# Kernel optimization log

Measured on AMD Instinct MI355X. Metric: run time of the kernel, lower is better.

Reference implementation:

```python
import jax, jax.numpy as jnp
import numpy as np
from jax.ops import segment_sum

B = 4096      # graphs per side (= batch of triples)
NPG = 32      # nodes per graph
N = B * NPG   # total nodes per batched graph
EPG = 128     # edges per graph
E = B * EPG   # total edges per batched graph
D = 256       # emb_dim
D4 = D // 4   # gnn1 out dim


def setup_inputs() -> dict:
    key = jax.random.key(0)
    ks = jax.random.split(key, 16)
    base = jnp.repeat(jnp.arange(B, dtype=jnp.int32) * NPG, EPG)  # graph offsets per edge
    def edges(k1, k2):
        s = base + jax.random.randint(k1, (E,), 0, NPG, dtype=jnp.int32)
        d = base + jax.random.randint(k2, (E,), 0, NPG, dtype=jnp.int32)
        return s, d
    subj_src, subj_dst = edges(ks[0], ks[1])
    obj_src, obj_dst = edges(ks[2], ks[3])
    node_graph_ids = jnp.repeat(jnp.arange(B, dtype=jnp.int32), NPG)
    # negative sampling indices (precomputed randomness, as in _sample_batch_negative_triples)
    head_or_tail = jax.random.randint(ks[4], (B,), 0, 2, dtype=jnp.int32)
    random_rows = jax.random.permutation(ks[5], B).astype(jnp.int32)
    ar = jnp.arange(B, dtype=jnp.int32)
    corrupt_hidx = jnp.where(head_or_tail == 1, random_rows, ar)
    corrupt_tidx = jnp.where(head_or_tail == 0, random_rows, ar)
    s = 0.02
    p = lambda k, sh: jax.random.normal(k, sh, dtype=jnp.float32) * s
    return {
        "subj_node_embs": jax.random.normal(ks[6], (N, D), dtype=jnp.float32),
        "obj_node_embs": jax.random.normal(ks[7], (N, D), dtype=jnp.float32),
        "rel_tok_embs": jax.random.normal(ks[8], (B, D), dtype=jnp.float32),
        "subj_src": subj_src, "subj_dst": subj_dst,
        "obj_src": obj_src, "obj_dst": obj_dst,
        "node_graph_ids": node_graph_ids,
        "corrupt_hidx": corrupt_hidx, "corrupt_tidx": corrupt_tidx,
        "WO1": p(ks[9], (D4, D)), "bO1": jnp.zeros((D4,), jnp.float32),
        "WI1": p(ks[10], (D4, D)), "bI1": jnp.zeros((D4,), jnp.float32),
        "WO2": p(ks[11], (D, D4)), "bO2": jnp.zeros((D,), jnp.float32),
        "WI2": p(ks[12], (D, D4)), "bI2": jnp.zeros((D,), jnp.float32),
        "relW": p(ks[13], (D, D)), "relb": jnp.zeros((D,), jnp.float32),
    }


def _mean_agg(h, idx_from, idx_to, n):
    # mean over edges (idx_from -> idx_to) of h[idx_from], per destination node; 0 for isolated
    deg = segment_sum(jnp.ones((idx_from.shape[0],), h.dtype), idx_to, num_segments=n)
    s = segment_sum(jnp.take(h, idx_from, axis=0), idx_to, num_segments=n)
    return s / jnp.maximum(deg, 1.0)[:, None]


def _compgcn(src, dst, h, WO, bO, WI, bI):
    n = h.shape[0]
    ho = _mean_agg(h, src, dst, n)   # forward graph: mean of in-neighbor sources
    hi = _mean_agg(h, dst, src, n)   # reversed graph: mean of out-neighbor targets
    return (ho @ WO.T + bO) + (hi @ WI.T + bI)


def _graph_emb(src, dst, node_embs, gids, WO1, bO1, WI1, bI1, WO2, bO2, WI2, bI2):
    hn = jax.nn.relu(_compgcn(src, dst, node_embs, WO1, bO1, WI1, bI1))
    hn = jax.nn.relu(_compgcn(src, dst, hn, WO2, bO2, WI2, bI2))
    # mean readout per graph
    cnt = segment_sum(jnp.ones((hn.shape[0],), hn.dtype), gids, num_segments=B)
    return segment_sum(hn, gids, num_segments=B) / cnt[:, None]


def _dist(h, r, t):
    return jnp.linalg.norm(h + r - t, ord=2, axis=1)


def reference(subj_node_embs, obj_node_embs, rel_tok_embs,
              subj_src, subj_dst, obj_src, obj_dst, node_graph_ids,
              corrupt_hidx, corrupt_tidx,
              WO1, bO1, WI1, bI1, WO2, bO2, WI2, bI2, relW, relb):
    h_embs = _graph_emb(subj_src, subj_dst, subj_node_embs, node_graph_ids,
                        WO1, bO1, WI1, bI1, WO2, bO2, WI2, bI2)
    t_embs = _graph_emb(obj_src, obj_dst, obj_node_embs, node_graph_ids,
                        WO1, bO1, WI1, bI1, WO2, bO2, WI2, bI2)
    r_embs = jax.nn.relu(rel_tok_embs @ relW.T + relb)
    pos_scores = _dist(h_embs, r_embs, t_embs)
    neg_scores = _dist(h_embs[corrupt_hidx], r_embs, t_embs[corrupt_tidx])
    return pos_scores, neg_scores
```

## Files before the change

kernel.cpp:

```cpp
#include <hip/hip_runtime.h>
#include <hip/hip_bf16.h>

#define BGR 4096
#define DIM 256
#define NGPB 8
#define HS  257

typedef __bf16 bf16x8 __attribute__((ext_vector_type(8)));
typedef __bf16 bf16x4 __attribute__((ext_vector_type(4)));
typedef float  f32x4  __attribute__((ext_vector_type(4)));

typedef const __attribute__((address_space(1))) unsigned int* gas_u32p;
typedef __attribute__((address_space(3))) unsigned int* las_u32p;

__device__ __forceinline__ unsigned short f2b(float f) {
  unsigned u = __builtin_bit_cast(unsigned, f);
  u = (u + 0x7FFFu + ((u >> 16) & 1u)) >> 16;
  return (unsigned short)u;
}

__device__ __forceinline__ bf16x8 cvt8(float4 a, float4 b) {
  bf16x8 r;
  r[0] = (__bf16)a.x; r[1] = (__bf16)a.y; r[2] = (__bf16)a.z; r[3] = (__bf16)a.w;
  r[4] = (__bf16)b.x; r[5] = (__bf16)b.y; r[6] = (__bf16)b.z; r[7] = (__bf16)b.w;
  return r;
}
__device__ __forceinline__ bf16x4 cvt4(f32x4 c) {
  bf16x4 r;
  r[0] = (__bf16)c[0]; r[1] = (__bf16)c[1]; r[2] = (__bf16)c[2]; r[3] = (__bf16)c[3];
  return r;
}

__global__ void wcvt_kernel(
    const float* __restrict__ WO1, const float* __restrict__ WI1,
    const float* __restrict__ WO2, const float* __restrict__ WI2,
    const float* __restrict__ bO1, const float* __restrict__ bI1,
    const float* __restrict__ bO2, const float* __restrict__ bI2,
    unsigned short* __restrict__ W1b, unsigned short* __restrict__ W2b,
    float* __restrict__ b1, float* __restrict__ b2)
{
  const int i = blockIdx.x * 256 + threadIdx.x;
  { int j = i >> 8, k = i & 255;
    float v = (j < 64) ? WO1[j * 256 + k] : WI1[(j - 64) * 256 + k];
    W1b[i] = f2b(v); }
  { int j = i >> 7, k = i & 127;
    float v = (k < 64) ? WO2[j * 64 + k] : WI2[j * 64 + (k - 64)];
    W2b[i] = f2b(v); }
  if (i < 64)  b1[i] = bO1[i] + bI1[i];
  if (i < 256) b2[i] = bO2[i] + bI2[i];
}

__global__ __launch_bounds__(256)
__attribute__((amdgpu_waves_per_eu(1, 2)))
void gemm0_kernel(
    const float* __restrict__ subj, const float* __restrict__ obj,
    const unsigned short* __restrict__ W1b, unsigned short* __restrict__ Yt)
{
  __shared__ __align__(16) float S[2][32 * 256];
  const int t = threadIdx.x, w = t >> 6, l = t & 63;
  const int ln16 = l & 15, kg = l >> 4;
  const int gid0 = blockIdx.x * NGPB;

  auto STAGE = [&](int g, int buf) {
    const int gid = gid0 + g;
    const float* Eg = ((gid >> 12) ? obj : subj) + (size_t)(gid & (BGR - 1)) * 32 * DIM;
    #pragma unroll
    for (int i = 0; i < 8; i++) {
      const int r = w * 8 + i;
      const float* src = Eg + r * 256 + ((l ^ i) << 2);
      __builtin_amdgcn_global_load_lds((gas_u32p)(const void*)src,
                                       (las_u32p)(void*)(&S[buf][r * 256]), 16, 0, 0);
    }
  };

  STAGE(0, 0);
  bf16x8 B0[8], B1[8];
  {
    const unsigned short* wb0 = W1b + ((2 * w) * 16 + ln16) * 256 + kg * 8;
    const unsigned short* wb1 = W1b + ((2 * w + 1) * 16 + ln16) * 256 + kg * 8;
    #pragma unroll
    for (int ks = 0; ks < 8; ks++) {
      B0[ks] = *(const bf16x8*)(wb0 + ks * 32);
      B1[ks] = *(const bf16x8*)(wb1 + ks * 32);
    }
  }
  STAGE(1, 1);

  #pragma unroll
  for (int g = 0; g < NGPB; g++) {
    if (g + 1 < NGPB) { asm volatile("s_waitcnt vmcnt(8)" ::: "memory"); }
    else              { asm volatile("s_waitcnt vmcnt(0)" ::: "memory"); }
    __builtin_amdgcn_s_barrier();
    __builtin_amdgcn_sched_barrier(0);

    const float* eb = &S[g & 1][0];
    const int swz = ln16 & 7;
    f32x4 a00 = {0,0,0,0}, a01 = {0,0,0,0}, a10 = {0,0,0,0}, a11 = {0,0,0,0};
    #pragma unroll
    for (int ks = 0; ks < 8; ks++) {
      const int c0 = ks * 8 + kg * 2;
      float4 lo0 = *(const float4*)(eb + ln16 * 256 + ((c0 ^ swz) << 2));
      float4 hi0 = *(const float4*)(eb + ln16 * 256 + (((c0 + 1) ^ swz) << 2));
      bf16x8 A0 = cvt8(lo0, hi0);
      a00 = __builtin_amdgcn_mfma_f32_16x16x32_bf16(A0, B0[ks], a00, 0, 0, 0);
      a01 = __builtin_amdgcn_mfma_f32_16x16x32_bf16(A0, B1[ks], a01, 0, 0, 0);
      float4 lo1 = *(const float4*)(eb + (16 + ln16) * 256 + ((c0 ^ swz) << 2));
      float4 hi1 = *(const float4*)(eb + (16 + ln16) * 256 + (((c0 + 1) ^ swz) << 2));
      bf16x8 A1 = cvt8(lo1, hi1);
      a10 = __builtin_amdgcn_mfma_f32_16x16x32_bf16(A1, B0[ks], a10, 0, 0, 0);
      a11 = __builtin_amdgcn_mfma_f32_16x16x32_bf16(A1, B1[ks], a11, 0, 0, 0);
    }
    {
      const int gid = gid0 + g;
      unsigned short* yo = Yt + (size_t)gid * 4096 + kg * 4;
      *(bf16x4*)(yo + ((2 * w) * 16 + ln16) * 32)          = cvt4(a00);
      *(bf16x4*)(yo + ((2 * w + 1) * 16 + ln16) * 32)      = cvt4(a01);
      *(bf16x4*)(yo + ((2 * w) * 16 + ln16) * 32 + 16)     = cvt4(a10);
      *(bf16x4*)(yo + ((2 * w + 1) * 16 + ln16) * 32 + 16) = cvt4(a11);
    }

    __builtin_amdgcn_sched_barrier(0);
    __builtin_amdgcn_s_barrier();
    __builtin_amdgcn_sched_barrier(0);
    if (g + 2 < NGPB) STAGE(g + 2, g & 1);
  }
}

__global__ __launch_bounds__(256)
__attribute__((amdgpu_waves_per_eu(2, 3)))
void graph_bc_kernel(
    const unsigned short* __restrict__ Yt,
    const int* __restrict__ ssrc, const int* __restrict__ sdst,
    const int* __restrict__ osrc, const int* __restrict__ odst,
    const unsigned short* __restrict__ W2b,
    const float* __restrict__ b1, const float* __restrict__ b2,
    float* __restrict__ gout)
{
  __shared__ __align__(16) unsigned char S[53248];
  const int t = threadIdx.x, w = t >> 6, l = t & 63;
  const int ln16 = l & 15, kg = l >> 4;
  const int gid = blockIdx.x * 4 + w;
  const int side = gid >> 12, g = gid & (BGR - 1);
  unsigned char* h1t = S + w * 13312;
  unsigned char* a2  = S + w * 13312 + 4608;
  unsigned* cw = (unsigned*)a2;

  const int* __restrict__ srcp = side ? osrc : ssrc;
  const int* __restrict__ dstp = side ? odst : sdst;

  const int eb = g * 128 + l;
  const int s0 = srcp[eb] & 31, s1 = srcp[eb + 64] & 31;
  const int d0 = dstp[eb] & 31, d1 = dstp[eb + 64] & 31;

  const unsigned short* yg = Yt + (size_t)gid * 4096;
  bf16x8 Bo[4], Bi[4];
  #pragma unroll
  for (int nt = 0; nt < 4; nt++) {
    Bo[nt] = *(const bf16x8*)(yg + (nt * 16 + ln16) * 32 + kg * 8);
    Bi[nt] = *(const bf16x8*)(yg + (64 + nt * 16 + ln16) * 32 + kg * 8);
  }
  float b1j[4];
  #pragma unroll
  for (int nt = 0; nt < 4; nt++) b1j[nt] = b1[nt * 16 + ln16];

  #pragma unroll
  for (int i = 0; i < 5; i++) cw[l + i * 64] = 0u;
  atomicAdd(&cw[d0 * 8 + (s0 >> 2)], 1u << ((s0 & 3) * 8));
  atomicAdd(&cw[d1 * 8 + (s1 >> 2)], 1u << ((s1 & 3) * 8));
  atomicAdd(&cw[256 + d0], 1u); atomicAdd(&cw[256 + d1], 1u);
  atomicAdd(&cw[288 + s0], 1u); atomicAdd(&cw[288 + s1], 1u);

  bf16x8 m1f[2], m2f[2];
  #pragma unroll
  for (int hf = 0; hf < 2; hf++) {
    const int r = hf * 16 + ln16;
    const float fi = 1.0f / fmaxf((float)cw[256 + r], 1.0f);
    const float fo = 1.0f / fmaxf((float)cw[288 + r], 1.0f);
    const unsigned w0 = cw[r * 8 + kg * 2], w1 = cw[r * 8 + kg * 2 + 1];
    bf16x8 a, b;
    #pragma unroll
    for (int q = 0; q < 4; q++) {
      a[q]     = (__bf16)((float)((w0 >> (q * 8)) & 255u) * fi);
      a[4 + q] = (__bf16)((float)((w1 >> (q * 8)) & 255u) * fi);
    }
    #pragma unroll
    for (int q = 0; q < 8; q++) {
      const unsigned wq = cw[(kg * 8 + q) * 8 + (r >> 2)];
      b[q] = (__bf16)((float)((wq >> ((r & 3) * 8)) & 255u) * fo);
    }
    m1f[hf] = a; m2f[hf] = b;
  }

  #pragma unroll
  for (int mt = 0; mt < 2; mt++)
    #pragma unroll
    for (int nt = 0; nt < 4; nt++) {
      f32x4 z = {0.f, 0.f, 0.f, 0.f};
      f32x4 c = __builtin_amdgcn_mfma_f32_16x16x32_bf16(m1f[mt], Bo[nt], z, 0, 0, 0);
      c = __builtin_amdgcn_mfma_f32_16x16x32_bf16(m2f[mt], Bi[nt], c, 0, 0, 0);
      f32x4 hv = { fmaxf(c[0] + b1j[nt], 0.f), fmaxf(c[1] + b1j[nt], 0.f),
                   fmaxf(c[2] + b1j[nt], 0.f), fmaxf(c[3] + b1j[nt], 0.f) };
      *(bf16x4*)(h1t + (nt * 16 + ln16) * 72 + (mt * 16 + kg * 4) * 2) = cvt4(hv);
    }

  #pragma unroll
  for (int mta = 0; mta < 4; mta++) {
    bf16x8 Af = *(const bf16x8*)(h1t + (mta * 16 + ln16) * 72 + kg * 16);
    #pragma unroll
    for (int hf = 0; hf < 2; hf++)
      #pragma unroll
      for (int ntd = 0; ntd < 2; ntd++) {
        f32x4 z = {0.f, 0.f, 0.f, 0.f};
        f32x4 c = __builtin_amdgcn_mfma_f32_16x16x32_bf16(
            Af, hf ? m2f[ntd] : m1f[ntd], z, 0, 0, 0);
        *(bf16x4*)(a2 + (ntd * 16 + ln16) * 272 + hf * 128 + mta * 32 + kg * 8) = cvt4(c);
      }
  }

  bf16x8 BF[2][4];
  #pragma unroll
  for (int ntd = 0; ntd < 2; ntd++)
    #pragma unroll
    for (int ks = 0; ks < 4; ks++)
      BF[ntd][ks] = *(const bf16x8*)(a2 + (ntd * 16 + ln16) * 272 + ks * 64 + kg * 16);

  #pragma unroll
  for (int mt = 0; mt < 16; mt++) {
    bf16x8 AW[4];
    #pragma unroll
    for (int ks = 0; ks < 4; ks++)
      AW[ks] = *(const bf16x8*)(W2b + (mt * 16 + ln16) * 128 + ks * 32 + kg * 8);
    f32x4 a0 = {0.f, 0.f, 0.f, 0.f}, a1 = {0.f, 0.f, 0.f, 0.f};
    #pragma unroll
    for (int ks = 0; ks < 4; ks++) {
      a0 = __builtin_amdgcn_mfma_f32_16x16x32_bf16(AW[ks], BF[0][ks], a0, 0, 0, 0);
      a1 = __builtin_amdgcn_mfma_f32_16x16x32_bf16(AW[ks], BF[1][ks], a1, 0, 0, 0);
    }
    const float4 bb = *(const float4*)(b2 + mt * 16 + kg * 4);
    float v0 = fmaxf(a0[0] + bb.x, 0.f) + fmaxf(a1[0] + bb.x, 0.f);
    float v1 = fmaxf(a0[1] + bb.y, 0.f) + fmaxf(a1[1] + bb.y, 0.f);
    float v2 = fmaxf(a0[2] + bb.z, 0.f) + fmaxf(a1[2] + bb.z, 0.f);
    float v3 = fmaxf(a0[3] + bb.w, 0.f) + fmaxf(a1[3] + bb.w, 0.f);
    #pragma unroll
    for (int d = 1; d < 16; d <<= 1) {
      v0 += __shfl_xor(v0, d); v1 += __shfl_xor(v1, d);
      v2 += __shfl_xor(v2, d); v3 += __shfl_xor(v3, d);
    }
    if (ln16 == 0) {
      float4 o = { v0 * 0.03125f, v1 * 0.03125f, v2 * 0.03125f, v3 * 0.03125f };
      *(float4*)(gout + (size_t)gid * DIM + mt * 16 + kg * 4) = o;
    }
  }
}

__global__ __launch_bounds__(256, 4) void rel_kernel(
    const float* __restrict__ rel, const float* __restrict__ relW,
    const float* __restrict__ relb, float* __restrict__ r_out)
{
  __shared__ float srel[16 * HS];
  const int t = threadIdx.x;
  const int b0 = blockIdx.x << 4;
  #pragma unroll
  for (int i = 0; i < 4; i++) {
    int f = (i << 8) + t;
    int r = f >> 6, k4 = f & 63;
    float4 x = *(const float4*)(rel + (size_t)(b0 + r) * DIM + (k4 << 2));
    float* d = &srel[r * HS + (k4 << 2)];
    d[0] = x.x; d[1] = x.y; d[2] = x.z; d[3] = x.w;
  }
  __syncthreads();
  const int r = t & 15, jg = t >> 4;
  const float* pa = &srel[r * HS];
  const float* w = relW + (size_t)(jg * 16) * DIM;
  float acc[16];
  #pragma unroll
  for (int jj = 0; jj < 16; jj++) acc[jj] = 0.f;
  for (int k0 = 0; k0 < DIM; k0 += 16) {
    float a[16];
    #pragma unroll
    for (int u = 0; u < 16; u++) a[u] = pa[k0 + u];
    #pragma unroll
    for (int jj = 0; jj < 16; jj++) {
      const float* wr = w + jj * DIM + k0;
      #pragma unroll
      for (int u = 0; u < 16; u += 4) {
        float4 wv = *(const float4*)(wr + u);
        acc[jj] += a[u]*wv.x + a[u+1]*wv.y + a[u+2]*wv.z + a[u+3]*wv.w;
      }
    }
  }
  float* outp = r_out + (size_t)(b0 + r) * DIM + jg * 16;
  #pragma unroll
  for (int jj = 0; jj < 16; jj++) outp[jj] = fmaxf(acc[jj] + relb[jg * 16 + jj], 0.f);
}

__global__ __launch_bounds__(256) void dist_kernel(
    const float* __restrict__ hemb, const float* __restrict__ temb,
    const float* __restrict__ remb, const int* __restrict__ chx,
    const int* __restrict__ ctx, float* __restrict__ out)
{
  const int t = threadIdx.x;
  const int w = t >> 6, l = t & 63;
  const int b = (blockIdx.x << 2) + w;
  float4 h4 = *(const float4*)(hemb + (size_t)b * DIM + (l << 2));
  float4 r4 = *(const float4*)(remb + (size_t)b * DIM + (l << 2));
  float4 t4 = *(const float4*)(temb + (size_t)b * DIM + (l << 2));
  int hb = chx[b], tb = ctx[b];
  float4 hn = *(const float4*)(hemb + (size_t)hb * DIM + (l << 2));
  float4 tn = *(const float4*)(temb + (size_t)tb * DIM + (l << 2));
  float x0 = h4.x + r4.x - t4.x, x1 = h4.y + r4.y - t4.y;
  float x2 = h4.z + r4.z - t4.z, x3 = h4.w + r4.w - t4.w;
  float dp = x0*x0 + x1*x1 + x2*x2 + x3*x3;
  float y0 = hn.x + r4.x - tn.x, y1 = hn.y + r4.y - tn.y;
  float y2 = hn.z + r4.z - tn.z, y3 = hn.w + r4.w - tn.w;
  float dn = y0*y0 + y1*y1 + y2*y2 + y3*y3;
  #pragma unroll
  for (int off = 32; off >= 1; off >>= 1) {
    dp += __shfl_down(dp, off);
    dn += __shfl_down(dn, off);
  }
  if (l == 0) {
    out[b] = sqrtf(dp);
    out[BGR + b] = sqrtf(dn);
  }
}

extern "C" void kernel_launch(void* const* d_in, const int* in_sizes, int n_in,
                              void* d_out, int out_size, void* d_ws, size_t ws_size,
                              hipStream_t stream) {
  const float* subj_embs = (const float*)d_in[0];
  const float* obj_embs  = (const float*)d_in[1];
  const float* rel_tok   = (const float*)d_in[2];
  const int* subj_src = (const int*)d_in[3];
  const int* subj_dst = (const int*)d_in[4];
  const int* obj_src  = (const int*)d_in[5];
  const int* obj_dst  = (const int*)d_in[6];
  const int* chx = (const int*)d_in[8];
  const int* ctx = (const int*)d_in[9];
  const float* WO1 = (const float*)d_in[10];
  const float* bO1 = (const float*)d_in[11];
  const float* WI1 = (const float*)d_in[12];
  const float* bI1 = (const float*)d_in[13];
  const float* WO2 = (const float*)d_in[14];
  const float* bO2 = (const float*)d_in[15];
  const float* WI2 = (const float*)d_in[16];
  const float* bI2 = (const float*)d_in[17];
  const float* relW = (const float*)d_in[18];
  const float* relb = (const float*)d_in[19];

  float* g_embs = (float*)d_ws;
  float* r_embs = g_embs + (size_t)2 * BGR * DIM;
  unsigned short* W1b = (unsigned short*)((char*)d_ws + 12582912);
  unsigned short* W2b = W1b + 32768;
  float* b1 = (float*)((char*)d_ws + 12713984);
  float* b2 = b1 + 64;
  unsigned short* Yt = (unsigned short*)((char*)d_ws + 16777216);
  float* out = (float*)d_out;

  wcvt_kernel<<<128, 256, 0, stream>>>(WO1, WI1, WO2, WI2, bO1, bI1, bO2, bI2,
                                       W1b, W2b, b1, b2);
  gemm0_kernel<<<1024, 256, 0, stream>>>(subj_embs, obj_embs, W1b, Yt);
  graph_bc_kernel<<<2048, 256, 0, stream>>>(
      Yt, subj_src, subj_dst, obj_src, obj_dst, W2b, b1, b2, g_embs);
  rel_kernel<<<BGR / 16, 256, 0, stream>>>(rel_tok, relW, relb, r_embs);
  dist_kernel<<<BGR / 4, 256, 0, stream>>>(
      g_embs, g_embs + (size_t)BGR * DIM, r_embs, chx, ctx, out);
}
```

Before: 217.3 us.

## Replace persistent double-buffered gemm0 with one-graph-per-block launch

Drops the software-pipelined loop in which each block processed 8 graphs with double-buffered LDS staging. Each block now handles a single graph with one LDS buffer, the grid grows to 8192 blocks, and the waves-per-EU hint is relaxed. The aim is to hide memory latency through higher occupancy and more blocks in flight rather than explicit prefetch. In exchange, every block reloads the W1 fragments into registers and pays its own launch and sync overhead.

```diff
diff --git a/kernel.cpp b/kernel.cpp
--- a/kernel.cpp
+++ b/kernel.cpp
@@ -3,7 +3,6 @@
 
 #define BGR 4096
 #define DIM 256
-#define NGPB 8
 #define HS  257
 
 typedef __bf16 bf16x8 __attribute__((ext_vector_type(8)));
@@ -51,29 +50,25 @@
 }
 
 __global__ __launch_bounds__(256)
-__attribute__((amdgpu_waves_per_eu(1, 2)))
+__attribute__((amdgpu_waves_per_eu(1, 5)))
 void gemm0_kernel(
     const float* __restrict__ subj, const float* __restrict__ obj,
     const unsigned short* __restrict__ W1b, unsigned short* __restrict__ Yt)
 {
-  __shared__ __align__(16) float S[2][32 * 256];
+  __shared__ __align__(16) float S[32 * 256];
   const int t = threadIdx.x, w = t >> 6, l = t & 63;
   const int ln16 = l & 15, kg = l >> 4;
-  const int gid0 = blockIdx.x * NGPB;
-
-  auto STAGE = [&](int g, int buf) {
-    const int gid = gid0 + g;
-    const float* Eg = ((gid >> 12) ? obj : subj) + (size_t)(gid & (BGR - 1)) * 32 * DIM;
-    #pragma unroll
-    for (int i = 0; i < 8; i++) {
-      const int r = w * 8 + i;
-      const float* src = Eg + r * 256 + ((l ^ i) << 2);
-      __builtin_amdgcn_global_load_lds((gas_u32p)(const void*)src,
-                                       (las_u32p)(void*)(&S[buf][r * 256]), 16, 0, 0);
-    }
-  };
-
-  STAGE(0, 0);
+  const int gid = blockIdx.x;
+  const float* Eg = ((gid >> 12) ? obj : subj) + (size_t)(gid & (BGR - 1)) * 32 * DIM;
+
+  #pragma unroll
+  for (int i = 0; i < 8; i++) {
+    const int r = w * 8 + i;
+    const float* src = Eg + r * 256 + ((l ^ i) << 2);
+    __builtin_amdgcn_global_load_lds((gas_u32p)(const void*)src,
+                                     (las_u32p)(void*)(&S[r * 256]), 16, 0, 0);
+  }
+
   bf16x8 B0[8], B1[8];
   {
     const unsigned short* wb0 = W1b + ((2 * w) * 16 + ln16) * 256 + kg * 8;
@@ -84,46 +79,29 @@
       B1[ks] = *(const bf16x8*)(wb1 + ks * 32);
     }
   }
-  STAGE(1, 1);
-
-  #pragma unroll
-  for (int g = 0; g < NGPB; g++) {
-    if (g + 1 < NGPB) { asm volatile("s_waitcnt vmcnt(8)" ::: "memory"); }
-    else              { asm volatile("s_waitcnt vmcnt(0)" ::: "memory"); }
-    __builtin_amdgcn_s_barrier();
-    __builtin_amdgcn_sched_barrier(0);
-
-    const float* eb = &S[g & 1][0];
-    const int swz = ln16 & 7;
-    f32x4 a00 = {0,0,0,0}, a01 = {0,0,0,0}, a10 = {0,0,0,0}, a11 = {0,0,0,0};
-    #pragma unroll
-    for (int ks = 0; ks < 8; ks++) {
-      const int c0 = ks * 8 + kg * 2;
-      float4 lo0 = *(const float4*)(eb + ln16 * 256 + ((c0 ^ swz) << 2));
-      float4 hi0 = *(const float4*)(eb + ln16 * 256 + (((c0 + 1) ^ swz) << 2));
-      bf16x8 A0 = cvt8(lo0, hi0);
-      a00 = __builtin_amdgcn_mfma_f32_16x16x32_bf16(A0, B0[ks], a00, 0, 0, 0);
-      a01 = __builtin_amdgcn_mfma_f32_16x16x32_bf16(A0, B1[ks], a01, 0, 0, 0);
-      float4 lo1 = *(const float4*)(eb + (16 + ln16) * 256 + ((c0 ^ swz) << 2));
-      float4 hi1 = *(const float4*)(eb + (16 + ln16) * 256 + (((c0 + 1) ^ swz) << 2));
-      bf16x8 A1 = cvt8(lo1, hi1);
-      a10 = __builtin_amdgcn_mfma_f32_16x16x32_bf16(A1, B0[ks], a10, 0, 0, 0);
-      a11 = __builtin_amdgcn_mfma_f32_16x16x32_bf16(A1, B1[ks], a11, 0, 0, 0);
-    }
-    {
-      const int gid = gid0 + g;
-      unsigned short* yo = Yt + (size_t)gid * 4096 + kg * 4;
-      *(bf16x4*)(yo + ((2 * w) * 16 + ln16) * 32)          = cvt4(a00);
-      *(bf16x4*)(yo + ((2 * w + 1) * 16 + ln16) * 32)      = cvt4(a01);
-      *(bf16x4*)(yo + ((2 * w) * 16 + ln16) * 32 + 16)     = cvt4(a10);
-      *(bf16x4*)(yo + ((2 * w + 1) * 16 + ln16) * 32 + 16) = cvt4(a11);
-    }
-
-    __builtin_amdgcn_sched_barrier(0);
-    __builtin_amdgcn_s_barrier();
-    __builtin_amdgcn_sched_barrier(0);
-    if (g + 2 < NGPB) STAGE(g + 2, g & 1);
-  }
+  __syncthreads();
+
+  const int swz = ln16 & 7;
+  f32x4 a00 = {0,0,0,0}, a01 = {0,0,0,0}, a10 = {0,0,0,0}, a11 = {0,0,0,0};
+  #pragma unroll
+  for (int ks = 0; ks < 8; ks++) {
+    const int c0 = ks * 8 + kg * 2;
+    float4 lo0 = *(const float4*)(&S[ln16 * 256 + ((c0 ^ swz) << 2)]);
+    float4 hi0 = *(const float4*)(&S[ln16 * 256 + (((c0 + 1) ^ swz) << 2)]);
+    bf16x8 A0 = cvt8(lo0, hi0);
+    a00 = __builtin_amdgcn_mfma_f32_16x16x32_bf16(A0, B0[ks], a00, 0, 0, 0);
+    a01 = __builtin_amdgcn_mfma_f32_16x16x32_bf16(A0, B1[ks], a01, 0, 0, 0);
+    float4 lo1 = *(const float4*)(&S[(16 + ln16) * 256 + ((c0 ^ swz) << 2)]);
+    float4 hi1 = *(const float4*)(&S[(16 + ln16) * 256 + (((c0 + 1) ^ swz) << 2)]);
+    bf16x8 A1 = cvt8(lo1, hi1);
+    a10 = __builtin_amdgcn_mfma_f32_16x16x32_bf16(A1, B0[ks], a10, 0, 0, 0);
+    a11 = __builtin_amdgcn_mfma_f32_16x16x32_bf16(A1, B1[ks], a11, 0, 0, 0);
+  }
+  unsigned short* yo = Yt + (size_t)gid * 4096 + kg * 4;
+  *(bf16x4*)(yo + ((2 * w) * 16 + ln16) * 32)          = cvt4(a00);
+  *(bf16x4*)(yo + ((2 * w + 1) * 16 + ln16) * 32)      = cvt4(a01);
+  *(bf16x4*)(yo + ((2 * w) * 16 + ln16) * 32 + 16)     = cvt4(a10);
+  *(bf16x4*)(yo + ((2 * w + 1) * 16 + ln16) * 32 + 16) = cvt4(a11);
 }
 
 __global__ __launch_bounds__(256)
@@ -359,7 +337,7 @@
 
   wcvt_kernel<<<128, 256, 0, stream>>>(WO1, WI1, WO2, WI2, bO1, bI1, bO2, bI2,
                                        W1b, W2b, b1, b2);
-  gemm0_kernel<<<1024, 256, 0, stream>>>(subj_embs, obj_embs, W1b, Yt);
+  gemm0_kernel<<<8192, 256, 0, stream>>>(subj_embs, obj_embs, W1b, Yt);
   graph_bc_kernel<<<2048, 256, 0, stream>>>(
       Yt, subj_src, subj_dst, obj_src, obj_dst, W2b, b1, b2, g_embs);
   rel_kernel<<<BGR / 16, 256, 0, stream>>>(rel_tok, relW, relb, r_embs);
```

New measurement: 238.5 us. +9.7%, slower.
